# Performance work log

Hardware: AMD Instinct MI355X
Metric: run time of the kernel (lower is better)

Reference implementation:

```python
import jax, jax.numpy as jnp
import numpy as np

EPS_LN = 1e-12   # BERT layer_norm_eps
EPS_COS = 1e-8   # torch.cosine_similarity eps


def _layernorm(x, g, b):
    m = x.mean(-1, keepdims=True)
    v = ((x - m) ** 2).mean(-1, keepdims=True)
    return (x - m) / jnp.sqrt(v + EPS_LN) * g + b


def setup_inputs() -> dict:
    B, L, H = 16, 512, 768
    S1, S2, NS = 32, 128, 8  # multi_explanation M = S1 // NS = 4
    ks = jax.random.split(jax.random.key(0), 12)
    hidden_states = jax.random.normal(ks[0], (B, L, H), jnp.float32)
    sent_h1 = jax.random.normal(ks[1], (B, L, H), jnp.float32)
    sent_h2 = jax.random.normal(ks[2], (B, L, H), jnp.float32)
    attention_mask = jax.random.randint(ks[3], (B, L), 0, 2, jnp.int32).at[:, 0].set(1)
    expl_h1 = jax.random.normal(ks[4], (B * S1, S2, H), jnp.float32)
    expl_h2 = jax.random.normal(ks[5], (B * S1, S2, H), jnp.float32)
    extra_attention_mask = jax.random.randint(ks[6], (B, S1, S2), 0, 2, jnp.int32).at[:, :, 0].set(1)
    extra_index = jax.random.randint(ks[7], (B, NS), 1, 5, jnp.int32)  # ragged group sizes in [1, M]
    extra_start = jax.random.randint(ks[8], (B,), 0, L // 2, jnp.int32)
    extra_end = extra_start + jax.random.randint(ks[9], (B,), 1, L // 2, jnp.int32)
    W_attn = jax.random.normal(ks[10], (H, H), jnp.float32) * 0.02
    W_t = jax.random.normal(ks[11], (H, H), jnp.float32) * 0.02
    b_t = jnp.zeros((H,), jnp.float32)
    gamma_t = jnp.ones((H,), jnp.float32)
    beta_t = jnp.zeros((H,), jnp.float32)
    gamma_s = jnp.ones((H,), jnp.float32)
    beta_s = jnp.zeros((H,), jnp.float32)
    return dict(hidden_states=hidden_states, sent_h1=sent_h1, sent_h2=sent_h2,
                attention_mask=attention_mask, expl_h1=expl_h1, expl_h2=expl_h2,
                extra_attention_mask=extra_attention_mask, extra_index=extra_index,
                extra_start=extra_start, extra_end=extra_end,
                W_attn=W_attn, W_t=W_t, b_t=b_t,
                gamma_t=gamma_t, beta_t=beta_t, gamma_s=gamma_s, beta_s=beta_s)


def reference(hidden_states, sent_h1, sent_h2, attention_mask, expl_h1, expl_h2,
              extra_attention_mask, extra_index, extra_start, extra_end,
              W_attn, W_t, b_t, gamma_t, beta_t, gamma_s, beta_s):
    B, L, H = hidden_states.shape
    _, NS = extra_index.shape
    _, S1, S2 = extra_attention_mask.shape
    M = S1 // NS  # multi_explanation

    # per-explanation-row masked mean pooling of (hidden_states[-1] + hidden_states[-2])
    expl_h = expl_h1 + expl_h2                                   # [B*S1, S2, H]
    am = extra_attention_mask.reshape(B * S1, S2).astype(expl_h.dtype)
    row_cls = jnp.einsum('ijk,ij->ik', expl_h, am) / am.sum(1, keepdims=True)  # [B*S1, H]
    cls = row_cls.reshape(B, NS, M, H)
    valid = jnp.arange(M)[None, None, :] < extra_index[:, :, None]  # [B, NS, M]

    # sentence pooling of input sequence
    iam = attention_mask.astype(expl_h.dtype)
    sp = jnp.einsum('blh,bl->bh', sent_h1 + sent_h2, iam) / iam.sum(1, keepdims=True)

    # ragged attention pooling over each group of M candidates (mask out invalid rows)
    sim = jnp.einsum('bd,dh,bnmh->bnm', sp, W_attn, cls) / jnp.sqrt(jnp.asarray(H, cls.dtype))
    w = jax.nn.softmax(jnp.where(valid, sim, -1e30), axis=-1)
    pooled = jnp.einsum('bnm,bnmh->bnh', w, cls)                 # [B, NS, H]

    # transform = Linear + LayerNorm
    cls_output = _layernorm(pooled @ W_t.T + b_t, gamma_t, beta_t)  # [B, NS, H]

    # selected span mean over hidden_states[i, start:end]
    pos = jnp.arange(L)
    smask = ((pos[None, :] >= extra_start[:, None]) & (pos[None, :] < extra_end[:, None])).astype(hidden_states.dtype)
    sel = jnp.einsum('blh,bl->bh', hidden_states, smask) / smask.sum(1, keepdims=True)
    sel = _layernorm(sel, gamma_s, beta_s)                        # [B, H]

    # torch.cosine_similarity default dim=1 (over the samples axis) -> [B, H]
    sel3 = jnp.broadcast_to(sel[:, None, :], cls_output.shape)
    num = (sel3 * cls_output).sum(axis=1)
    n1 = jnp.sqrt((sel3 ** 2).sum(axis=1))
    n2 = jnp.sqrt((cls_output ** 2).sum(axis=1))
    score = num / (jnp.maximum(n1, EPS_COS) * jnp.maximum(n2, EPS_COS))
    return score
```

## Files before the change

### kernel.cpp

```cpp
#include <hip/hip_runtime.h>
#include <math.h>

#define B   16
#define L   512
#define H   768
#define HV4 192
#define S1  32
#define S2  128
#define NS  8
#define M   4
#define CH  16
#define NCHUNK 32

__global__ __launch_bounds__(384)
void k_pool(const float* __restrict__ e1, const float* __restrict__ e2,
            const int* __restrict__ am,
            const float* __restrict__ s1, const float* __restrict__ s2,
            const int* __restrict__ iam,
            const float* __restrict__ hs, const int* __restrict__ st_,
            const int* __restrict__ en_,
            float* __restrict__ row_cls,
            float* __restrict__ sp_part, float* __restrict__ sp_cnt,
            float* __restrict__ sel_part, float* __restrict__ sel_cnt) {
  const int bid = blockIdx.x;
  const int t = threadIdx.x;
  const int half = t / 192;
  const int tt = t % 192;
  __shared__ int   idxL[S2];
  __shared__ int   cntS;
  __shared__ float4 pf[192];

  if (bid < 512) {
    const int i = bid;
    if (t < 64) {
      const int m0 = am[i * S2 + t];
      const int m1 = am[i * S2 + 64 + t];
      const unsigned long long b0 = __ballot(m0 != 0);
      const unsigned long long b1 = __ballot(m1 != 0);
      const int c0 = (int)__popcll(b0);
      if (m0) idxL[(int)__popcll(b0 & ((1ULL << t) - 1))] = t;
      if (m1) idxL[c0 + (int)__popcll(b1 & ((1ULL << t) - 1))] = 64 + t;
      if (t == 0) cntS = c0 + (int)__popcll(b1);
    }
    __syncthreads();
    const int cnt = cntS;
    const int cntH = (cnt + 1 - half) >> 1;
    const float4* p1 = (const float4*)e1 + (size_t)i * (S2 * HV4) + tt;
    const float4* p2 = (const float4*)e2 + (size_t)i * (S2 * HV4) + tt;
    float ax = 0.f, ay = 0.f, az = 0.f, aw = 0.f;
    int kk = 0;
    for (; kk + 3 < cntH; kk += 4) {
      const int j0 = idxL[2 * kk + half];
      const int j1 = idxL[2 * (kk + 1) + half];
      const int j2 = idxL[2 * (kk + 2) + half];
      const int j3 = idxL[2 * (kk + 3) + half];
      float4 a0 = p1[j0 * HV4], b0 = p2[j0 * HV4];
      float4 a1 = p1[j1 * HV4], b1 = p2[j1 * HV4];
      float4 a2 = p1[j2 * HV4], b2 = p2[j2 * HV4];
      float4 a3 = p1[j3 * HV4], b3 = p2[j3 * HV4];
      ax += (a0.x + b0.x) + (a1.x + b1.x) + (a2.x + b2.x) + (a3.x + b3.x);
      ay += (a0.y + b0.y) + (a1.y + b1.y) + (a2.y + b2.y) + (a3.y + b3.y);
      az += (a0.z + b0.z) + (a1.z + b1.z) + (a2.z + b2.z) + (a3.z + b3.z);
      aw += (a0.w + b0.w) + (a1.w + b1.w) + (a2.w + b2.w) + (a3.w + b3.w);
    }
    for (; kk < cntH; ++kk) {
      const int j = idxL[2 * kk + half];
      float4 a = p1[j * HV4], b = p2[j * HV4];
      ax += a.x + b.x; ay += a.y + b.y; az += a.z + b.z; aw += a.w + b.w;
    }
    if (half == 1) { float4 o; o.x = ax; o.y = ay; o.z = az; o.w = aw; pf[tt] = o; }
    __syncthreads();
    if (half == 0) {
      const float inv = 1.f / (float)cnt;
      float4 o = pf[tt];
      o.x = (ax + o.x) * inv; o.y = (ay + o.y) * inv;
      o.z = (az + o.z) * inv; o.w = (aw + o.w) * inv;
      ((float4*)row_cls)[(size_t)i * HV4 + tt] = o;
    }
  } else if (bid < 1024) {
    const int blk = bid - 512;
    const int b = blk >> 5, c = blk & 31;
    if (t < 64) {
      const int m = (t < CH) ? iam[b * L + c * CH + t] : 0;
      const unsigned long long bm = __ballot(m != 0);
      if (m) idxL[(int)__popcll(bm & ((1ULL << t) - 1))] = t;
      if (t == 0) { const int cc = (int)__popcll(bm); cntS = cc; sp_cnt[blk] = (float)cc; }
    }
    __syncthreads();
    const int cnt = cntS;
    const int cntH = (cnt + 1 - half) >> 1;
    const float4* p1 = (const float4*)s1 + ((size_t)b * L + c * CH) * HV4 + tt;
    const float4* p2 = (const float4*)s2 + ((size_t)b * L + c * CH) * HV4 + tt;
    float ax = 0.f, ay = 0.f, az = 0.f, aw = 0.f;
    int kk = 0;
    for (; kk + 1 < cntH; kk += 2) {
      const int l0 = idxL[2 * kk + half];
      const int l1 = idxL[2 * (kk + 1) + half];
      float4 a0 = p1[l0 * HV4], b0 = p2[l0 * HV4];
      float4 a1 = p1[l1 * HV4], b1 = p2[l1 * HV4];
      ax += (a0.x + b0.x) + (a1.x + b1.x);
      ay += (a0.y + b0.y) + (a1.y + b1.y);
      az += (a0.z + b0.z) + (a1.z + b1.z);
      aw += (a0.w + b0.w) + (a1.w + b1.w);
    }
    for (; kk < cntH; ++kk) {
      const int l = idxL[2 * kk + half];
      float4 a = p1[l * HV4], b = p2[l * HV4];
      ax += a.x + b.x; ay += a.y + b.y; az += a.z + b.z; aw += a.w + b.w;
    }
    if (half == 1) { float4 o; o.x = ax; o.y = ay; o.z = az; o.w = aw; pf[tt] = o; }
    __syncthreads();
    if (half == 0) {
      float4 o = pf[tt];
      o.x += ax; o.y += ay; o.z += az; o.w += aw;
      ((float4*)sp_part)[(size_t)blk * HV4 + tt] = o;
    }
  } else {
    const int blk = bid - 1024;
    const int b = blk >> 5, c = blk & 31;
    const int st = st_[b], en = en_[b];
    const int lo = st > c * CH ? st : c * CH;
    const int hi = en < c * CH + CH ? en : c * CH + CH;
    const float4* p = (const float4*)hs + (size_t)b * L * HV4 + tt;
    float ax = 0.f, ay = 0.f, az = 0.f, aw = 0.f;
    for (int l = lo + half; l < hi; l += 2) {
      float4 a0 = p[l * HV4];
      ax += a0.x; ay += a0.y; az += a0.z; aw += a0.w;
    }
    if (half == 1) { float4 o; o.x = ax; o.y = ay; o.z = az; o.w = aw; pf[tt] = o; }
    __syncthreads();
    if (half == 0) {
      float4 o = pf[tt];
      o.x += ax; o.y += ay; o.z += az; o.w += aw;
      ((float4*)sel_part)[(size_t)blk * HV4 + tt] = o;
      if (tt == 0) sel_cnt[blk] = (float)(hi > lo ? hi - lo : 0);
    }
  }
}

__global__ __launch_bounds__(256)
void k_sp(const float* __restrict__ sp_part, const float* __restrict__ sp_cnt,
          const float* __restrict__ sel_part, const float* __restrict__ sel_cnt,
          const float* __restrict__ gamma_s, const float* __restrict__ beta_s,
          float* __restrict__ sp, float* __restrict__ sel_ln) {
  const int bid = blockIdx.x, t = threadIdx.x;
  const int lane = t & 63, w = t >> 6;
  __shared__ float red[8];
  if (bid < B) {
    const int b = bid;
    float csp = 0.f;
    for (int c = 0; c < NCHUNK; ++c) csp += sp_cnt[b * NCHUNK + c];
    const float inv = 1.f / csp;
    #pragma unroll
    for (int k = 0; k < 3; ++k) {
      const int h = t + k * 256;
      float a = 0.f;
      #pragma unroll
      for (int c = 0; c < NCHUNK; ++c)
        a += sp_part[((size_t)b * NCHUNK + c) * H + h];
      sp[(size_t)b * H + h] = a * inv;
    }
  } else {
    const int b = bid - B;
    float csel = 0.f;
    for (int c = 0; c < NCHUNK; ++c) csel += sel_cnt[b * NCHUNK + c];
    const float invc = 1.f / csel;
    float selv[3];
    #pragma unroll
    for (int k = 0; k < 3; ++k) {
      const int h = t + k * 256;
      float s = 0.f;
      #pragma unroll
      for (int c = 0; c < NCHUNK; ++c)
        s += sel_part[((size_t)b * NCHUNK + c) * H + h];
      selv[k] = s * invc;
    }
    float s = selv[0] + selv[1] + selv[2];
    float ss = selv[0] * selv[0] + selv[1] * selv[1] + selv[2] * selv[2];
    #pragma unroll
    for (int off = 32; off > 0; off >>= 1) {
      s += __shfl_down(s, off);
      ss += __shfl_down(ss, off);
    }
    if (lane == 0) { red[w] = s; red[4 + w] = ss; }
    __syncthreads();
    const float S = red[0] + red[1] + red[2] + red[3];
    const float SS = red[4] + red[5] + red[6] + red[7];
    const float mu = S / (float)H;
    const float var = SS / (float)H - mu * mu;
    const float rstd = rsqrtf(var + 1e-12f);
    #pragma unroll
    for (int k = 0; k < 3; ++k) {
      const int h = t + k * 256;
      sel_ln[(size_t)b * H + h] = (selv[k] - mu) * rstd * gamma_s[h] + beta_s[h];
    }
  }
}

__global__ __launch_bounds__(1024)
void k_mid_q(const float* __restrict__ sp, const float* __restrict__ W_attn,
             const float* __restrict__ rc, float* __restrict__ simp) {
  const int bid = blockIdx.x, t = threadIdx.x;
  const int b = bid / 12, ht = bid % 12;
  const int lane = t & 63, w = t >> 6;
  __shared__ float spL[H];
  __shared__ float red[1024];
  __shared__ float qt[64];
  if (t < H) spL[t] = sp[(size_t)b * H + t];
  __syncthreads();
  {
    const int h = ht * 64 + lane;
    const float* wp = W_attn + (size_t)(w * 48) * H + h;
    const float* sv = spL + w * 48;
    float acc = 0.f;
    #pragma unroll 8
    for (int i = 0; i < 48; ++i) acc += sv[i] * wp[(size_t)i * H];
    red[t] = acc;
  }
  __syncthreads();
  if (t < 64) {
    float a = 0.f;
    #pragma unroll
    for (int ww = 0; ww < 16; ++ww) a += red[ww * 64 + t];
    qt[t] = a;
  }
  __syncthreads();
  {
    const int i = t >> 5, sub = t & 31;
    const float* rr = rc + (size_t)(b * S1 + i) * H + ht * 64 + sub * 2;
    float p = qt[sub * 2] * rr[0] + qt[sub * 2 + 1] * rr[1];
    p += __shfl_down(p, 16);
    p += __shfl_down(p, 8);
    p += __shfl_down(p, 4);
    p += __shfl_down(p, 2);
    p += __shfl_down(p, 1);
    if (sub == 0) simp[((size_t)b * 12 + ht) * S1 + i] = p;
  }
}

__global__ __launch_bounds__(1024)
void k_attn_tr(const float* __restrict__ simp, const float* __restrict__ rc,
               const int* __restrict__ extra_index,
               const float* __restrict__ W_t, const float* __restrict__ b_t,
               float* __restrict__ yb) {
  const int bid = blockIdx.x, t = threadIdx.x;
  const int b = bid / 12, hc = bid % 12;
  const int lane = t & 63, w = t >> 6;
  __shared__ float pL[NS * H];
  __shared__ float simR[S1];
  __shared__ float w2L[S1];
  float4 wv[4][3];
  #pragma unroll
  for (int r = 0; r < 4; ++r) {
    const float4* wr = (const float4*)(W_t + (size_t)(hc * 64 + w * 4 + r) * H);
    wv[r][0] = wr[lane];
    wv[r][1] = wr[lane + 64];
    wv[r][2] = wr[lane + 128];
  }
  if (t < S1) {
    float a = 0.f;
    for (int ht = 0; ht < 12; ++ht)
      a += simp[((size_t)b * 12 + ht) * S1 + t];
    simR[t] = a;
  }
  __syncthreads();
  if (t < NS) {
    const int vid = extra_index[b * NS + t];
    const float scale = 0.036084391824351615f;
    float x[M], mx = -1e30f;
    #pragma unroll
    for (int m = 0; m < M; ++m) {
      x[m] = (m < vid) ? simR[t * M + m] * scale : -1e30f;
      mx = fmaxf(mx, x[m]);
    }
    float s = 0.f, e[M];
    #pragma unroll
    for (int m = 0; m < M; ++m) { e[m] = expf(x[m] - mx); s += e[m]; }
    #pragma unroll
    for (int m = 0; m < M; ++m) w2L[t * M + m] = e[m] / s;
  }
  __syncthreads();
  if (t < H) {
    const int d = t;
    #pragma unroll
    for (int n = 0; n < NS; ++n) {
      float p = 0.f;
      #pragma unroll
      for (int m = 0; m < M; ++m)
        p += w2L[n * M + m] * rc[(size_t)(b * S1 + n * M + m) * H + d];
      pL[n * H + d] = p;
    }
  }
  __syncthreads();
  float part[4][NS];
  #pragma unroll
  for (int n = 0; n < NS; ++n) {
    const float4* pq = (const float4*)(pL + n * H);
    const float4 p0 = pq[lane];
    const float4 p1 = pq[lane + 64];
    const float4 p2 = pq[lane + 128];
    #pragma unroll
    for (int r = 0; r < 4; ++r) {
      part[r][n] = wv[r][0].x * p0.x + wv[r][0].y * p0.y + wv[r][0].z * p0.z + wv[r][0].w * p0.w
                 + wv[r][1].x * p1.x + wv[r][1].y * p1.y + wv[r][1].z * p1.z + wv[r][1].w * p1.w
                 + wv[r][2].x * p2.x + wv[r][2].y * p2.y + wv[r][2].z * p2.z + wv[r][2].w * p2.w;
    }
  }
  #pragma unroll
  for (int off = 32; off > 0; off >>= 1) {
    #pragma unroll
    for (int r = 0; r < 4; ++r)
      #pragma unroll
      for (int n = 0; n < NS; ++n)
        part[r][n] += __shfl_down(part[r][n], off);
  }
  if (lane == 0) {
    #pragma unroll
    for (int r = 0; r < 4; ++r) {
      const int h = hc * 64 + w * 4 + r;
      const float bias = b_t[h];
      #pragma unroll
      for (int n = 0; n < NS; ++n)
        yb[((size_t)b * NS + n) * H + h] = part[r][n] + bias;
    }
  }
}

__global__ __launch_bounds__(256)
void k_lnscore(const float* __restrict__ yb, const float* __restrict__ gamma,
               const float* __restrict__ beta, const float* __restrict__ sel_ln,
               float* __restrict__ out) {
  const int b = blockIdx.x, t = threadIdx.x;
  const int lane = t & 63, w = t >> 6;
  __shared__ float redS[NS * 4];
  __shared__ float redQ[NS * 4];
  float v[NS][3];
  for (int n = 0; n < NS; ++n) {
    float s = 0.f, ss = 0.f;
    #pragma unroll
    for (int k = 0; k < 3; ++k) {
      const float x = yb[((size_t)b * NS + n) * H + t + k * 256];
      v[n][k] = x; s += x; ss += x * x;
    }
    #pragma unroll
    for (int off = 32; off > 0; off >>= 1) {
      s += __shfl_down(s, off);
      ss += __shfl_down(ss, off);
    }
    if (lane == 0) { redS[n * 4 + w] = s; redQ[n * 4 + w] = ss; }
  }
  __syncthreads();
  float g[3], be[3];
  #pragma unroll
  for (int k = 0; k < 3; ++k) { g[k] = gamma[t + k * 256]; be[k] = beta[t + k * 256]; }
  float S[3] = {0.f, 0.f, 0.f}, SS[3] = {0.f, 0.f, 0.f};
  for (int n = 0; n < NS; ++n) {
    const float Sn = redS[n * 4] + redS[n * 4 + 1] + redS[n * 4 + 2] + redS[n * 4 + 3];
    const float Qn = redQ[n * 4] + redQ[n * 4 + 1] + redQ[n * 4 + 2] + redQ[n * 4 + 3];
    const float mu = Sn / (float)H;
    const float var = Qn / (float)H - mu * mu;
    const float rstd = rsqrtf(var + 1e-12f);
    #pragma unroll
    for (int k = 0; k < 3; ++k) {
      const float c = (v[n][k] - mu) * rstd * g[k] + be[k];
      S[k] += c; SS[k] += c * c;
    }
  }
  #pragma unroll
  for (int k = 0; k < 3; ++k) {
    const int h = t + k * 256;
    const float sl = sel_ln[(size_t)b * H + h];
    const float n1 = 2.8284271247461903f * fabsf(sl);
    const float n2 = sqrtf(SS[k]);
    out[(size_t)b * H + h] = sl * S[k] / (fmaxf(n1, 1e-8f) * fmaxf(n2, 1e-8f));
  }
}

extern "C" void kernel_launch(void* const* d_in, const int* in_sizes, int n_in,
                              void* d_out, int out_size, void* d_ws, size_t ws_size,
                              hipStream_t stream) {
  const float* hidden_states = (const float*)d_in[0];
  const float* sent_h1       = (const float*)d_in[1];
  const float* sent_h2       = (const float*)d_in[2];
  const int*   attention_mask= (const int*)  d_in[3];
  const float* expl_h1       = (const float*)d_in[4];
  const float* expl_h2       = (const float*)d_in[5];
  const int*   extra_am      = (const int*)  d_in[6];
  const int*   extra_index   = (const int*)  d_in[7];
  const int*   extra_start   = (const int*)  d_in[8];
  const int*   extra_end     = (const int*)  d_in[9];
  const float* W_attn        = (const float*)d_in[10];
  const float* W_t           = (const float*)d_in[11];
  const float* b_t           = (const float*)d_in[12];
  const float* gamma_t       = (const float*)d_in[13];
  const float* beta_t        = (const float*)d_in[14];
  const float* gamma_s       = (const float*)d_in[15];
  const float* beta_s        = (const float*)d_in[16];
  float* out = (float*)d_out;

  float* ws = (float*)d_ws;
  float* row_cls  = ws;
  float* sp_part  = row_cls + 512 * H;
  float* sp_cnt   = sp_part + 512 * H;
  float* sel_part = sp_cnt + 512;
  float* sel_cnt  = sel_part + 512 * H;
  float* sel_ln   = sel_cnt + 512;
  float* sp       = sel_ln + B * H;
  float* simp     = sp + B * H;
  float* yb       = simp + B * 12 * S1;

  k_pool<<<1536, 384, 0, stream>>>(expl_h1, expl_h2, extra_am,
                                   sent_h1, sent_h2, attention_mask,
                                   hidden_states, extra_start, extra_end,
                                   row_cls, sp_part, sp_cnt, sel_part, sel_cnt);
  k_sp<<<32, 256, 0, stream>>>(sp_part, sp_cnt, sel_part, sel_cnt,
                               gamma_s, beta_s, sp, sel_ln);
  k_mid_q<<<192, 1024, 0, stream>>>(sp, W_attn, row_cls, simp);
  k_attn_tr<<<192, 1024, 0, stream>>>(simp, row_cls, extra_index, W_t, b_t, yb);
  k_lnscore<<<B, 256, 0, stream>>>(yb, gamma_t, beta_t, sel_ln, out);
}
```

Measured before the change: 74.05 us.

## Restructure attention and transform to read weight matrices once across batches

Replaces the per-batch q and pooling/transform kernels with a per-column-slice q kernel over all batches, a separate ragged attention-pooling kernel, and a transform kernel that stages all pooled rows in shared memory. The goal is to stop re-reading W_attn and W_t once per batch. In exchange the grid shrinks to 12 blocks for the matvec kernels, with long serial inner loops, and an extra kernel launch plus a pooled intermediate buffer are added.

Result: slower. 274.9 us (+271.2%).

```diff
diff --git a/kernel.cpp b/kernel.cpp
--- a/kernel.cpp
+++ b/kernel.cpp
@@ -198,131 +198,131 @@
 }
 
 __global__ __launch_bounds__(1024)
-void k_mid_q(const float* __restrict__ sp, const float* __restrict__ W_attn,
-             const float* __restrict__ rc, float* __restrict__ simp) {
-  const int bid = blockIdx.x, t = threadIdx.x;
-  const int b = bid / 12, ht = bid % 12;
+void k_q(const float* __restrict__ sp, const float* __restrict__ W_attn,
+         const float* __restrict__ rc, float* __restrict__ simp) {
+  const int ht = blockIdx.x, t = threadIdx.x;
   const int lane = t & 63, w = t >> 6;
-  __shared__ float spL[H];
-  __shared__ float red[1024];
-  __shared__ float qt[64];
-  if (t < H) spL[t] = sp[(size_t)b * H + t];
+  __shared__ float spL[B * H];
+  __shared__ float qL[B * 64];
+  {
+    float4* d4 = (float4*)spL;
+    const float4* s4 = (const float4*)sp;
+    #pragma unroll
+    for (int k = 0; k < 3; ++k) d4[t + k * 1024] = s4[t + k * 1024];
+  }
   __syncthreads();
   {
-    const int h = ht * 64 + lane;
-    const float* wp = W_attn + (size_t)(w * 48) * H + h;
-    const float* sv = spL + w * 48;
+    const float* sv = spL + w * H;
+    const float* wp = W_attn + ht * 64 + lane;
     float acc = 0.f;
     #pragma unroll 8
-    for (int i = 0; i < 48; ++i) acc += sv[i] * wp[(size_t)i * H];
-    red[t] = acc;
+    for (int d = 0; d < H; ++d) acc += sv[d] * wp[(size_t)d * H];
+    qL[w * 64 + lane] = acc;
   }
   __syncthreads();
-  if (t < 64) {
+  #pragma unroll 1
+  for (int pass = 0; pass < 32; ++pass) {
+    const int row = pass * 16 + w;
+    const int b = row >> 5, i = row & 31;
+    float p = rc[(size_t)row * H + ht * 64 + lane] * qL[b * 64 + lane];
+    p += __shfl_down(p, 32); p += __shfl_down(p, 16); p += __shfl_down(p, 8);
+    p += __shfl_down(p, 4);  p += __shfl_down(p, 2);  p += __shfl_down(p, 1);
+    if (lane == 0) simp[((size_t)b * 12 + ht) * S1 + i] = p;
+  }
+}
+
+__global__ __launch_bounds__(256)
+void k_attn_pool(const float* __restrict__ simp, const float* __restrict__ rc,
+                 const int* __restrict__ extra_index, float* __restrict__ pooled) {
+  const int bid = blockIdx.x, t = threadIdx.x;
+  const int b = bid >> 3, n = bid & 7;
+  __shared__ float simL[M];
+  __shared__ float wL[M];
+  if (t < M) {
     float a = 0.f;
     #pragma unroll
-    for (int ww = 0; ww < 16; ++ww) a += red[ww * 64 + t];
-    qt[t] = a;
+    for (int ht = 0; ht < 12; ++ht)
+      a += simp[((size_t)b * 12 + ht) * S1 + n * M + t];
+    simL[t] = a;
   }
   __syncthreads();
-  {
-    const int i = t >> 5, sub = t & 31;
-    const float* rr = rc + (size_t)(b * S1 + i) * H + ht * 64 + sub * 2;
-    float p = qt[sub * 2] * rr[0] + qt[sub * 2 + 1] * rr[1];
-    p += __shfl_down(p, 16);
-    p += __shfl_down(p, 8);
-    p += __shfl_down(p, 4);
-    p += __shfl_down(p, 2);
-    p += __shfl_down(p, 1);
-    if (sub == 0) simp[((size_t)b * 12 + ht) * S1 + i] = p;
+  if (t == 0) {
+    const int vid = extra_index[b * NS + n];
+    const float scale = 0.036084391824351615f;
+    float x[M], mx = -1e30f;
+    #pragma unroll
+    for (int m = 0; m < M; ++m) {
+      x[m] = (m < vid) ? simL[m] * scale : -1e30f;
+      mx = fmaxf(mx, x[m]);
+    }
+    float s = 0.f, e[M];
+    #pragma unroll
+    for (int m = 0; m < M; ++m) { e[m] = expf(x[m] - mx); s += e[m]; }
+    #pragma unroll
+    for (int m = 0; m < M; ++m) wL[m] = e[m] / s;
+  }
+  __syncthreads();
+  const float w0 = wL[0], w1 = wL[1], w2 = wL[2], w3 = wL[3];
+  const float* r0 = rc + (size_t)(b * S1 + n * M + 0) * H;
+  const float* r1 = rc + (size_t)(b * S1 + n * M + 1) * H;
+  const float* r2 = rc + (size_t)(b * S1 + n * M + 2) * H;
+  const float* r3 = rc + (size_t)(b * S1 + n * M + 3) * H;
+  #pragma unroll
+  for (int k = 0; k < 3; ++k) {
+    const int d = t + k * 256;
+    pooled[(size_t)bid * H + d] = w0 * r0[d] + w1 * r1[d] + w2 * r2[d] + w3 * r3[d];
   }
 }
 
 __global__ __launch_bounds__(1024)
-void k_attn_tr(const float* __restrict__ simp, const float* __restrict__ rc,
-               const int* __restrict__ extra_index,
-               const float* __restrict__ W_t, const float* __restrict__ b_t,
-               float* __restrict__ yb) {
-  const int bid = blockIdx.x, t = threadIdx.x;
-  const int b = bid / 12, hc = bid % 12;
+void k_transform(const float* __restrict__ pooled, const float* __restrict__ W_t,
+                 const float* __restrict__ b_t, float* __restrict__ yb) {
+  const int hc = blockIdx.x, t = threadIdx.x;
   const int lane = t & 63, w = t >> 6;
-  __shared__ float pL[NS * H];
-  __shared__ float simR[S1];
-  __shared__ float w2L[S1];
+  __shared__ float4 pooledL4[32 * HV4];
   float4 wv[4][3];
+  float bt[4];
   #pragma unroll
   for (int r = 0; r < 4; ++r) {
-    const float4* wr = (const float4*)(W_t + (size_t)(hc * 64 + w * 4 + r) * H);
+    const int h = hc * 64 + w * 4 + r;
+    const float4* wr = (const float4*)(W_t + (size_t)h * H);
     wv[r][0] = wr[lane];
     wv[r][1] = wr[lane + 64];
     wv[r][2] = wr[lane + 128];
-  }
-  if (t < S1) {
-    float a = 0.f;
-    for (int ht = 0; ht < 12; ++ht)
-      a += simp[((size_t)b * 12 + ht) * S1 + t];
-    simR[t] = a;
-  }
-  __syncthreads();
-  if (t < NS) {
-    const int vid = extra_index[b * NS + t];
-    const float scale = 0.036084391824351615f;
-    float x[M], mx = -1e30f;
-    #pragma unroll
-    for (int m = 0; m < M; ++m) {
-      x[m] = (m < vid) ? simR[t * M + m] * scale : -1e30f;
-      mx = fmaxf(mx, x[m]);
-    }
-    float s = 0.f, e[M];
-    #pragma unroll
-    for (int m = 0; m < M; ++m) { e[m] = expf(x[m] - mx); s += e[m]; }
-    #pragma unroll
-    for (int m = 0; m < M; ++m) w2L[t * M + m] = e[m] / s;
-  }
-  __syncthreads();
-  if (t < H) {
-    const int d = t;
-    #pragma unroll
-    for (int n = 0; n < NS; ++n) {
-      float p = 0.f;
+    bt[r] = b_t[h];
+  }
+  #pragma unroll 1
+  for (int c = 0; c < 4; ++c) {
+    const float4* src = (const float4*)pooled + (size_t)c * 32 * HV4;
+    #pragma unroll
+    for (int k = 0; k < 6; ++k) pooledL4[t + k * 1024] = src[t + k * 1024];
+    __syncthreads();
+    #pragma unroll 1
+    for (int p = 0; p < 32; ++p) {
+      const float4* pq = pooledL4 + p * HV4;
+      const float4 p0 = pq[lane];
+      const float4 p1 = pq[lane + 64];
+      const float4 p2 = pq[lane + 128];
+      float pr[4];
       #pragma unroll
-      for (int m = 0; m < M; ++m)
-        p += w2L[n * M + m] * rc[(size_t)(b * S1 + n * M + m) * H + d];
-      pL[n * H + d] = p;
-    }
-  }
-  __syncthreads();
-  float part[4][NS];
-  #pragma unroll
-  for (int n = 0; n < NS; ++n) {
-    const float4* pq = (const float4*)(pL + n * H);
-    const float4 p0 = pq[lane];
-    const float4 p1 = pq[lane + 64];
-    const float4 p2 = pq[lane + 128];
-    #pragma unroll
-    for (int r = 0; r < 4; ++r) {
-      part[r][n] = wv[r][0].x * p0.x + wv[r][0].y * p0.y + wv[r][0].z * p0.z + wv[r][0].w * p0.w
-                 + wv[r][1].x * p1.x + wv[r][1].y * p1.y + wv[r][1].z * p1.z + wv[r][1].w * p1.w
-                 + wv[r][2].x * p2.x + wv[r][2].y * p2.y + wv[r][2].z * p2.z + wv[r][2].w * p2.w;
-    }
-  }
-  #pragma unroll
-  for (int off = 32; off > 0; off >>= 1) {
-    #pragma unroll
-    for (int r = 0; r < 4; ++r)
+      for (int r = 0; r < 4; ++r) {
+        pr[r] = wv[r][0].x * p0.x + wv[r][0].y * p0.y + wv[r][0].z * p0.z + wv[r][0].w * p0.w
+              + wv[r][1].x * p1.x + wv[r][1].y * p1.y + wv[r][1].z * p1.z + wv[r][1].w * p1.w
+              + wv[r][2].x * p2.x + wv[r][2].y * p2.y + wv[r][2].z * p2.z + wv[r][2].w * p2.w;
+      }
       #pragma unroll
-      for (int n = 0; n < NS; ++n)
-        part[r][n] += __shfl_down(part[r][n], off);
-  }
-  if (lane == 0) {
-    #pragma unroll
-    for (int r = 0; r < 4; ++r) {
-      const int h = hc * 64 + w * 4 + r;
-      const float bias = b_t[h];
-      #pragma unroll
-      for (int n = 0; n < NS; ++n)
-        yb[((size_t)b * NS + n) * H + h] = part[r][n] + bias;
-    }
+      for (int off = 32; off > 0; off >>= 1) {
+        #pragma unroll
+        for (int r = 0; r < 4; ++r) pr[r] += __shfl_down(pr[r], off);
+      }
+      if (lane == 0) {
+        const int gp = c * 32 + p;
+        #pragma unroll
+        for (int r = 0; r < 4; ++r)
+          yb[(size_t)gp * H + hc * 64 + w * 4 + r] = pr[r] + bt[r];
+      }
+    }
+    __syncthreads();
   }
 }
 
@@ -407,7 +407,8 @@
   float* sel_ln   = sel_cnt + 512;
   float* sp       = sel_ln + B * H;
   float* simp     = sp + B * H;
-  float* yb       = simp + B * 12 * S1;
+  float* pooled   = simp + B * 12 * S1;
+  float* yb       = pooled + B * NS * H;
 
   k_pool<<<1536, 384, 0, stream>>>(expl_h1, expl_h2, extra_am,
                                    sent_h1, sent_h2, attention_mask,
@@ -415,7 +416,8 @@
                                    row_cls, sp_part, sp_cnt, sel_part, sel_cnt);
   k_sp<<<32, 256, 0, stream>>>(sp_part, sp_cnt, sel_part, sel_cnt,
                                gamma_s, beta_s, sp, sel_ln);
-  k_mid_q<<<192, 1024, 0, stream>>>(sp, W_attn, row_cls, simp);
-  k_attn_tr<<<192, 1024, 0, stream>>>(simp, row_cls, extra_index, W_t, b_t, yb);
+  k_q<<<12, 1024, 0, stream>>>(sp, W_attn, row_cls, simp);
+  k_attn_pool<<<128, 256, 0, stream>>>(simp, row_cls, extra_index, pooled);
+  k_transform<<<12, 1024, 0, stream>>>(pooled, W_t, b_t, yb);
   k_lnscore<<<B, 256, 0, stream>>>(yb, gamma_t, beta_t, sel_ln, out);
 }
```
